# Optimization experiments

Hardware: AMD Instinct MI355X
Metric: run time of the kernel (lower is better)

## Reference

```python
import jax, jax.numpy as jnp
import numpy as np

N_ROLES = 6
EPS = 1e-5

def _ln(x, scale, bias):
    m = jnp.mean(x, axis=-1, keepdims=True)
    v = jnp.var(x, axis=-1, keepdims=True)
    return (x - m) * jax.lax.rsqrt(v + EPS) * scale + bias

def setup_inputs() -> dict:
    key = jax.random.key(0)
    ks = jax.random.split(key, 20)
    T, B, D_OBS, H, A = 32, 1024, 256, 512, 32
    inp = {
        'rnn_states': jax.random.normal(ks[0], (B, H), jnp.float32),
        'obs': jax.random.normal(ks[1], (T, B, D_OBS), jnp.float32),
        'resets': jnp.zeros((T, B), jnp.float32),
        'available_actions': jnp.ones((T, B, A), jnp.float32),
        'role_ids': jax.random.randint(ks[2], (T, B), 0, N_ROLES, jnp.int32),
        # feature norm over obs_dim
        'fn_scale': jnp.ones((D_OBS,), jnp.float32),
        'fn_bias': jnp.zeros((D_OBS,), jnp.float32),
        # base MLP: obs_dim->512->512, each followed by LayerNorm
        'W0': jax.random.normal(ks[3], (D_OBS, H), jnp.float32) * 0.02,
        'b0': jnp.zeros((H,), jnp.float32),
        'ln0_scale': jnp.ones((H,), jnp.float32),
        'ln0_bias': jnp.zeros((H,), jnp.float32),
        'W1': jax.random.normal(ks[4], (H, H), jnp.float32) * 0.02,
        'b1': jnp.zeros((H,), jnp.float32),
        'ln1_scale': jnp.ones((H,), jnp.float32),
        'ln1_bias': jnp.zeros((H,), jnp.float32),
        # per-role routes: obs_dim->128->H (stacked over roles)
        'Wr0': jax.random.normal(ks[5], (N_ROLES, D_OBS, 128), jnp.float32) * 0.02,
        'br0': jnp.zeros((N_ROLES, 128), jnp.float32),
        'Wr1': jax.random.normal(ks[6], (N_ROLES, 128, H), jnp.float32) * 0.02,
        'br1': jnp.zeros((N_ROLES, H), jnp.float32),
        # per-role heads: H->64->32->action_dim (stacked over roles)
        'Wh0': jax.random.normal(ks[7], (N_ROLES, H, 64), jnp.float32) * 0.02,
        'bh0': jnp.zeros((N_ROLES, 64), jnp.float32),
        'Wh1': jax.random.normal(ks[8], (N_ROLES, 64, 32), jnp.float32) * 0.02,
        'bh1': jnp.zeros((N_ROLES, 32), jnp.float32),
        'Wh2': jax.random.normal(ks[9], (N_ROLES, 32, A), jnp.float32) * 0.02,
        'bh2': jnp.zeros((N_ROLES, A), jnp.float32),
    }
    return inp

def _gather_by_role(all_values, role_ids):
    # all_values: (K, T, B, F); role_ids: (T, B) -> (T, B, F)
    idx = role_ids[None, :, :, None].astype(jnp.int32)
    return jnp.take_along_axis(all_values, idx, axis=0)[0]

def reference(rnn_states, obs, resets, available_actions, role_ids,
              fn_scale, fn_bias, W0, b0, ln0_scale, ln0_bias,
              W1, b1, ln1_scale, ln1_bias,
              Wr0, br0, Wr1, br1,
              Wh0, bh0, Wh1, bh1, Wh2, bh2):
    # feature normalization on raw obs
    obs_n = _ln(obs, fn_scale, fn_bias)
    # shared base MLP (relu + LayerNorm after each Dense)
    e = _ln(jax.nn.relu(obs_n @ W0 + b0), ln0_scale, ln0_bias)
    e = _ln(jax.nn.relu(e @ W1 + b1), ln1_scale, ln1_bias)
    # per-role pre-GRU residual routes on (normalized) obs
    r = jax.nn.relu(jnp.einsum('tbi,kih->ktbh', obs_n, Wr0) + br0[:, None, None, :])
    r = jax.nn.relu(jnp.einsum('ktbh,kho->ktbo', r, Wr1) + br1[:, None, None, :])
    e = e + _gather_by_role(r, role_ids)
    # no recurrent policy configured: rnn_states pass through
    # per-role heads -> all logits (K, T, B, A)
    h = jax.nn.relu(jnp.einsum('tbh,khf->ktbf', e, Wh0) + bh0[:, None, None, :])
    h = jax.nn.relu(jnp.einsum('ktbf,kfg->ktbg', h, Wh1) + bh1[:, None, None, :])
    all_logits = jnp.einsum('ktbg,kga->ktba', h, Wh2) + bh2[:, None, None, :]
    logits = _gather_by_role(all_logits, role_ids)
    logits = jnp.where(available_actions > 0.5, logits, jnp.full_like(logits, -1e10))
    return rnn_states, logits
```

## Files before the change

kernel.cpp:

```cpp
#include <hip/hip_runtime.h>
#include <stdint.h>

typedef unsigned short u16;
typedef unsigned int u32;

using bf16x8 = __attribute__((ext_vector_type(8))) short;
using f32x4  = __attribute__((ext_vector_type(4))) float;

#define DEVINL __device__ __forceinline__

DEVINL float b2f(u16 u) { return __builtin_bit_cast(float, (u32)u << 16); }
DEVINL u16 f2b(float f) {
  u32 u = __builtin_bit_cast(u32, f);
  u += 0x7FFFu + ((u >> 16) & 1u);
  return (u16)(u >> 16);
}

DEVINL void gll16(const u16* src, u16* dst) {
  __builtin_amdgcn_global_load_lds(
      (const __attribute__((address_space(1))) void*)(uintptr_t)src,
      (__attribute__((address_space(3))) void*)(uintptr_t)dst, 16, 0, 0);
}

#define MFMA __builtin_amdgcn_mfma_f32_16x16x32_bf16

DEVINL void tp_tile(const float* __restrict__ s, u16* __restrict__ d,
                    int R, int C, int bx, int by, int z)
{
  __shared__ u16 tile[32][33];
  const size_t mstride = (size_t)R * C;
  s += (size_t)z * mstride;
  d += (size_t)z * mstride;
  int r0 = bx * 32, c0 = by * 32;
  int tx = threadIdx.x & 31, ty = threadIdx.x >> 5;
#pragma unroll
  for (int i = 0; i < 32; i += 8)
    tile[ty + i][tx] = f2b(s[(size_t)(r0 + ty + i) * C + (c0 + tx)]);
  __syncthreads();
#pragma unroll
  for (int i = 0; i < 32; i += 8)
    d[(size_t)(c0 + ty + i) * R + (r0 + tx)] = tile[tx][ty + i];
}

__global__ __launch_bounds__(256) void transpose_all(
    const float* W0, const float* W1, const float* Wr0, const float* Wr1, const float* Wh0,
    u16* W0t, u16* W1t, u16* Wr0t, u16* Wr1t, u16* Wh0t)
{
  int b = blockIdx.x;
  if (b < 128)      {            tp_tile(W0, W0t, 256, 512, b % 8,  b / 8, 0); }
  else if (b < 384) { b -= 128;  tp_tile(W1, W1t, 512, 512, b % 16, b / 16, 0); }
  else if (b < 576) { b -= 384;  int t = b / 8;  tp_tile(Wr0, Wr0t, 256, 128, b % 8,  t % 4,  t / 4); }
  else if (b < 960) { b -= 576;  int t = b / 4;  tp_tile(Wr1, Wr1t, 128, 512, b % 4,  t % 16, t / 16); }
  else              { b -= 960;  int t = b / 16; tp_tile(Wh0, Wh0t, 512, 64,  b % 16, t % 2,  t / 2); }
}

__global__ __launch_bounds__(256) void ln_f32_256(
    const float* __restrict__ X, const float* __restrict__ sc,
    const float* __restrict__ bi, u16* __restrict__ Y, int nrows)
{
  constexpr int D = 256, PER = 4;
  int lane = threadIdx.x & 63;
  int row = blockIdx.x * 4 + (threadIdx.x >> 6);
  if (row >= nrows) return;
  const float* xr = X + (size_t)row * D + lane * PER;
  float x[PER] __attribute__((aligned(16)));
  *(float4*)x = *(const float4*)xr;
  float s = 0.f, s2 = 0.f;
#pragma unroll
  for (int p = 0; p < PER; ++p) { s += x[p]; s2 += x[p] * x[p]; }
#pragma unroll
  for (int o = 32; o > 0; o >>= 1) { s += __shfl_xor(s, o, 64); s2 += __shfl_xor(s2, o, 64); }
  float m = s * (1.f / D);
  float v = s2 * (1.f / D) - m * m;
  float inv = rsqrtf(v + 1e-5f);
  u16 yu[PER] __attribute__((aligned(8)));
#pragma unroll
  for (int p = 0; p < PER; ++p)
    yu[p] = f2b((x[p] - m) * inv * sc[lane * PER + p] + bi[lane * PER + p]);
  *(uint2*)(Y + (size_t)row * D + lane * PER) = *(uint2*)yu;
}

#define NROLE 6
__global__ __launch_bounds__(256) void role_count(
    const int* __restrict__ rid, int* __restrict__ blkCnt)
{
  __shared__ int h[NROLE];
  if (threadIdx.x < NROLE) h[threadIdx.x] = 0;
  __syncthreads();
  int i = blockIdx.x * 256 + threadIdx.x;
  atomicAdd(&h[rid[i]], 1);
  __syncthreads();
  if (threadIdx.x < NROLE) blkCnt[blockIdx.x * NROLE + threadIdx.x] = h[threadIdx.x];
}

__global__ __launch_bounds__(256) void role_scan(
    const int* __restrict__ blkCnt, int* __restrict__ blkBase,
    int* __restrict__ baseArr, int* __restrict__ cntArr)
{
  __shared__ int c[128 * NROLE];
  __shared__ int bb[128 * NROLE];
  __shared__ int sbase[NROLE], scnt[NROLE];
  for (int i = threadIdx.x; i < 128 * NROLE; i += 256) c[i] = blkCnt[i];
  __syncthreads();
  if (threadIdx.x < NROLE) {
    int k = threadIdx.x, run = 0;
    for (int b = 0; b < 128; ++b) { bb[b * NROLE + k] = run; run += c[b * NROLE + k]; }
    scnt[k] = run;
  }
  __syncthreads();
  if (threadIdx.x == 0) {
    int r = 0;
    for (int k = 0; k < NROLE; ++k) { sbase[k] = r; r += scnt[k]; }
  }
  __syncthreads();
  if (threadIdx.x < NROLE) { baseArr[threadIdx.x] = sbase[threadIdx.x]; cntArr[threadIdx.x] = scnt[threadIdx.x]; }
  for (int i = threadIdx.x; i < 128 * NROLE; i += 256)
    blkBase[i] = bb[i] + sbase[i % NROLE];
}

__global__ __launch_bounds__(256) void role_fill(
    const int* __restrict__ rid, const int* __restrict__ blkBase, int* __restrict__ bucket)
{
  __shared__ int h[NROLE];
  if (threadIdx.x < NROLE) h[threadIdx.x] = 0;
  __syncthreads();
  int i = blockIdx.x * 256 + threadIdx.x;
  int k = rid[i];
  int pos = atomicAdd(&h[k], 1);
  bucket[blkBase[blockIdx.x * NROLE + k] + pos] = i;
}

template <int K>
__global__ __launch_bounds__(256, 2) void gemm_ln(
    const u16* __restrict__ A, const u16* __restrict__ Bt,
    const float* __restrict__ bias, const float* __restrict__ lnsc,
    const float* __restrict__ lnbi, u16* __restrict__ C)
{
  constexpr int BK = 64, NI = K / BK;
  __shared__ __align__(16) u16 As[2][64 * BK];
  __shared__ float redS[64][4];
  __shared__ float redSS[64][4];
  __shared__ float prm[1536];
  const int tid = threadIdx.x;
  const int rowBase = blockIdx.x * 64;
  const int lane = tid & 63, wave = tid >> 6;
#pragma unroll
  for (int i = tid; i < 512; i += 256) {
    prm[i] = bias[i]; prm[512 + i] = lnsc[i]; prm[1024 + i] = lnbi[i];
  }
  u32 aOff[2];
#pragma unroll
  for (int r = 0; r < 2; ++r) {
    int row = r * 32 + (tid >> 3);
    aOff[r] = (u32)(rowBase + row) * (u32)K + (u32)(((tid & 7) ^ (row & 7)) * 8);
  }
  const int quad = lane >> 4, lm = lane & 15, l7 = lm & 7;
  const int wn = wave * 128;
  u32 bOff[8];
#pragma unroll
  for (int j = 0; j < 8; ++j)
    bOff[j] = (u32)(wn + j * 16 + lm) * (u32)K + (u32)(quad * 8);

  f32x4 acc[4][8] = {};

#pragma unroll
  for (int r = 0; r < 2; ++r)
    gll16(A + aOff[r], &As[0][r * 2048 + wave * 512]);
  bf16x8 bP[8];
#pragma unroll
  for (int j = 0; j < 8; ++j)
    bP[j] = *(const bf16x8*)(Bt + bOff[j]);
  __syncthreads();

  for (int i = 0; i < NI; ++i) {
    const u16* Ab = As[i & 1];
    if (i + 1 < NI) {
#pragma unroll
      for (int r = 0; r < 2; ++r)
        gll16(A + aOff[r] + (i + 1) * BK, &As[(i + 1) & 1][r * 2048 + wave * 512]);
    }
    bf16x8 bN[8];
#pragma unroll
    for (int j = 0; j < 8; ++j)
      bN[j] = *(const bf16x8*)(Bt + bOff[j] + i * BK + 32);
    bf16x8 af[4];
#pragma unroll
    for (int i2 = 0; i2 < 4; ++i2)
      af[i2] = *(const bf16x8*)&Ab[(i2 * 16 + lm) * 64 + ((quad ^ l7) * 8)];
#pragma unroll
    for (int i2 = 0; i2 < 4; ++i2)
#pragma unroll
      for (int j = 0; j < 8; ++j)
        acc[i2][j] = MFMA(af[i2], bP[j], acc[i2][j], 0, 0, 0);
    if (i + 1 < NI) {
#pragma unroll
      for (int j = 0; j < 8; ++j)
        bP[j] = *(const bf16x8*)(Bt + bOff[j] + (i + 1) * BK);
    }
#pragma unroll
    for (int i2 = 0; i2 < 4; ++i2)
      af[i2] = *(const bf16x8*)&Ab[(i2 * 16 + lm) * 64 + (((quad + 4) ^ l7) * 8)];
#pragma unroll
    for (int i2 = 0; i2 < 4; ++i2)
#pragma unroll
      for (int j = 0; j < 8; ++j)
        acc[i2][j] = MFMA(af[i2], bN[j], acc[i2][j], 0, 0, 0);
    __syncthreads();
  }

#pragma unroll
  for (int i2 = 0; i2 < 4; ++i2) {
#pragma unroll
    for (int r2 = 0; r2 < 4; ++r2) {
      float s = 0.f, ss = 0.f;
#pragma unroll
      for (int j = 0; j < 8; ++j) {
        float v = fmaxf(acc[i2][j][r2] + prm[wn + j * 16 + lm], 0.f);
        acc[i2][j][r2] = v;
        s += v; ss += v * v;
      }
#pragma unroll
      for (int o = 1; o < 16; o <<= 1) { s += __shfl_xor(s, o, 64); ss += __shfl_xor(ss, o, 64); }
      if (lm == 0) {
        int rowL = i2 * 16 + quad * 4 + r2;
        redS[rowL][wave] = s;
        redSS[rowL][wave] = ss;
      }
    }
  }
  __syncthreads();
#pragma unroll
  for (int i2 = 0; i2 < 4; ++i2) {
#pragma unroll
    for (int r2 = 0; r2 < 4; ++r2) {
      int rowL = i2 * 16 + quad * 4 + r2;
      float ts  = redS[rowL][0] + redS[rowL][1] + redS[rowL][2] + redS[rowL][3];
      float tss = redSS[rowL][0] + redSS[rowL][1] + redSS[rowL][2] + redSS[rowL][3];
      float m = ts * (1.f / 512.f);
      float var = tss * (1.f / 512.f) - m * m;
      float inv = rsqrtf(var + 1e-5f);
      size_t base = (size_t)(rowBase + rowL) * 512;
#pragma unroll
      for (int j = 0; j < 8; ++j) {
        int col = wn + j * 16 + lm;
        float y = (acc[i2][j][r2] - m) * inv * prm[512 + col] + prm[1024 + col];
        C[base + col] = f2b(y);
      }
    }
  }
}

__global__ __launch_bounds__(256, 2) void route_head(
    const u16* __restrict__ obs_n, const u16* __restrict__ e,
    const u16* __restrict__ Wr0t, const float* __restrict__ br0,
    const u16* __restrict__ Wr1t, const float* __restrict__ br1,
    const u16* __restrict__ Wh0t, const float* __restrict__ bh0,
    const float* __restrict__ Wh1, const float* __restrict__ bh1,
    const float* __restrict__ Wh2, const float* __restrict__ bh2,
    const float* __restrict__ avail,
    const int* __restrict__ bucket, const int* __restrict__ baseArr,
    const int* __restrict__ cntArr, float* __restrict__ outLogits)
{
  __shared__ __align__(16) u16 sm[28672];
  __shared__ float prm[704];
  __shared__ float h1s[32 * 36];
  const int tid = threadIdx.x;

  int role = 0, rem = blockIdx.x, cnt;
  for (;;) {
    cnt = cntArr[role];
    int tiles = (cnt + 31) >> 5;
    if (rem < tiles) break;
    rem -= tiles;
    if (++role >= NROLE) return;
  }
  const int limit = cnt;
  const int rowBase = rem * 32;
  const int roleBase = baseArr[role];

  const int lane = tid & 63, wave = tid >> 6;
  const int quad = lane >> 4, lm = lane & 15, l7 = lm & 7;

#pragma unroll
  for (int r = 0; r < 4; ++r) {
    int lrow = r * 8 + (tid >> 5);
    int i = rowBase + lrow;
    if (i >= limit) i = rowBase;
    int grow = bucket[roleBase + i];
    gll16(obs_n + (u32)grow * 256u + (u32)(((tid & 31) ^ (lrow & 7)) * 8),
          &sm[16384 + r * 2048 + wave * 512]);
  }
#pragma unroll
  for (int r = 0; r < 8; ++r) {
    int lrow = r * 4 + wave;
    int i = rowBase + lrow;
    if (i >= limit) i = rowBase;
    int grow = bucket[roleBase + i];
    int chunk = tid & 63;
    int sw = (chunk & 56) | ((chunk ^ lrow) & 7);
    gll16(e + (u32)grow * 512u + (u32)(sw * 8),
          &sm[r * 2048 + wave * 512]);
  }
  {
    if (tid < 128) prm[tid] = br0[role * 128 + tid];
    for (int i = tid; i < 512; i += 256) prm[128 + i] = br1[role * 512 + i];
    if (tid < 64) prm[640 + tid] = bh0[role * 64 + tid];
  }
  __syncthreads();

  const int wn0 = wave * 32;
  const u16* B0 = Wr0t + (size_t)role * 128 * 256;
  f32x4 acc0[2][2] = {};
  bf16x8 b0P[2];
#pragma unroll
  for (int j = 0; j < 2; ++j)
    b0P[j] = *(const bf16x8*)(B0 + (u32)(wn0 + j * 16 + lm) * 256u + (u32)(quad * 8));
#pragma unroll
  for (int kk = 0; kk < 256; kk += 32) {
    bf16x8 b0N[2];
    if (kk + 32 < 256) {
#pragma unroll
      for (int j = 0; j < 2; ++j)
        b0N[j] = *(const bf16x8*)(B0 + (u32)(wn0 + j * 16 + lm) * 256u + (u32)(quad * 8 + kk + 32));
    }
    const int kc = kk >> 3;
    bf16x8 af[2];
#pragma unroll
    for (int i2 = 0; i2 < 2; ++i2)
      af[i2] = *(const bf16x8*)&sm[16384 + (i2 * 16 + lm) * 256 + (((quad + kc) ^ l7) * 8)];
#pragma unroll
    for (int i2 = 0; i2 < 2; ++i2)
#pragma unroll
      for (int j = 0; j < 2; ++j)
        acc0[i2][j] = MFMA(af[i2], b0P[j], acc0[i2][j], 0, 0, 0);
    if (kk + 32 < 256) { b0P[0] = b0N[0]; b0P[1] = b0N[1]; }
  }
  u16* r1 = sm + 24576;
#pragma unroll
  for (int i2 = 0; i2 < 2; ++i2) {
#pragma unroll
    for (int r2 = 0; r2 < 4; ++r2) {
      int row = i2 * 16 + quad * 4 + r2;
#pragma unroll
      for (int j = 0; j < 2; ++j) {
        int col = wn0 + j * 16 + lm;
        float v = fmaxf(acc0[i2][j][r2] + prm[col], 0.f);
        r1[row * 128 + (((col >> 3) ^ (row & 7)) * 8) + (col & 7)] = f2b(v);
      }
    }
  }
  __syncthreads();

  const int wn1 = wave * 128;
  const u16* B1 = Wr1t + (size_t)role * 512 * 128;
  f32x4 acc1[2][8] = {};
  bf16x8 b1P[8];
#pragma unroll
  for (int j = 0; j < 8; ++j)
    b1P[j] = *(const bf16x8*)(B1 + (u32)(wn1 + j * 16 + lm) * 128u + (u32)(quad * 8));
#pragma unroll
  for (int kk = 0; kk < 128; kk += 32) {
    bf16x8 b1N[8];
    if (kk + 32 < 128) {
#pragma unroll
      for (int j = 0; j < 8; ++j)
        b1N[j] = *(const bf16x8*)(B1 + (u32)(wn1 + j * 16 + lm) * 128u + (u32)(quad * 8 + kk + 32));
    }
    const int kc = kk >> 3;
    bf16x8 af[2];
#pragma unroll
    for (int i2 = 0; i2 < 2; ++i2)
      af[i2] = *(const bf16x8*)&r1[(i2 * 16 + lm) * 128 + (((quad + kc) ^ l7) * 8)];
#pragma unroll
    for (int i2 = 0; i2 < 2; ++i2)
#pragma unroll
      for (int j = 0; j < 8; ++j)
        acc1[i2][j] = MFMA(af[i2], b1P[j], acc1[i2][j], 0, 0, 0);
    if (kk + 32 < 128) {
#pragma unroll
      for (int j = 0; j < 8; ++j) b1P[j] = b1N[j];
    }
  }
#pragma unroll
  for (int i2 = 0; i2 < 2; ++i2) {
#pragma unroll
    for (int r2 = 0; r2 < 4; ++r2) {
      int row = i2 * 16 + quad * 4 + r2;
#pragma unroll
      for (int j = 0; j < 8; ++j) {
        int col = wn1 + j * 16 + lm;
        int addr = row * 512 + (((col >> 3) ^ (row & 7)) * 8) + (col & 7);
        float v = fmaxf(acc1[i2][j][r2] + prm[128 + col], 0.f) + b2f(sm[addr]);
        sm[addr] = f2b(v);
      }
    }
  }
  __syncthreads();

  const int wn2 = wave * 16;
  const u16* B2 = Wh0t + (size_t)role * 64 * 512;
  f32x4 acc2[2] = {};
  bf16x8 b2P = *(const bf16x8*)(B2 + (u32)(wn2 + lm) * 512u + (u32)(quad * 8));
#pragma unroll
  for (int kk = 0; kk < 512; kk += 32) {
    bf16x8 b2N;
    if (kk + 32 < 512)
      b2N = *(const bf16x8*)(B2 + (u32)(wn2 + lm) * 512u + (u32)(quad * 8 + kk + 32));
    const int kc = kk >> 3;
    bf16x8 af[2];
#pragma unroll
    for (int i2 = 0; i2 < 2; ++i2)
      af[i2] = *(const bf16x8*)&sm[(i2 * 16 + lm) * 512 + (((quad + kc) ^ l7) * 8)];
#pragma unroll
    for (int i2 = 0; i2 < 2; ++i2)
      acc2[i2] = MFMA(af[i2], b2P, acc2[i2], 0, 0, 0);
    if (kk + 32 < 512) b2P = b2N;
  }
  u16* h0s = sm + 16384;
#pragma unroll
  for (int i2 = 0; i2 < 2; ++i2) {
#pragma unroll
    for (int r2 = 0; r2 < 4; ++r2) {
      int row = i2 * 16 + quad * 4 + r2;
      int col = wn2 + lm;
      h0s[row * 68 + col] = f2b(fmaxf(acc2[i2][r2] + prm[640 + col], 0.f));
    }
  }
  __syncthreads();

  {
    const int r = tid >> 3;
    const int n0 = (tid & 7) * 4;
    const bool valid = (rowBase + r) < limit;
    const float* W1k = Wh1 + (size_t)role * 64 * 32;
    const float* W2k = Wh2 + (size_t)role * 32 * 32;
    float4 a1 = *(const float4*)(bh1 + role * 32 + n0);
#pragma unroll 8
    for (int j = 0; j < 64; ++j) {
      float hj = b2f(h0s[r * 68 + j]);
      float4 wv = *(const float4*)(W1k + j * 32 + n0);
      a1.x += hj * wv.x; a1.y += hj * wv.y; a1.z += hj * wv.z; a1.w += hj * wv.w;
    }
    h1s[r * 36 + n0 + 0] = fmaxf(a1.x, 0.f);
    h1s[r * 36 + n0 + 1] = fmaxf(a1.y, 0.f);
    h1s[r * 36 + n0 + 2] = fmaxf(a1.z, 0.f);
    h1s[r * 36 + n0 + 3] = fmaxf(a1.w, 0.f);
    __syncthreads();
    float4 a2 = *(const float4*)(bh2 + role * 32 + n0);
#pragma unroll 8
    for (int n = 0; n < 32; ++n) {
      float hn = h1s[r * 36 + n];
      float4 wv = *(const float4*)(W2k + n * 32 + n0);
      a2.x += hn * wv.x; a2.y += hn * wv.y; a2.z += hn * wv.z; a2.w += hn * wv.w;
    }
    if (valid) {
      int g = bucket[roleBase + rowBase + r];
      float4 av = *(const float4*)(avail + (size_t)g * 32 + n0);
      float4 o;
      o.x = (av.x > 0.5f) ? a2.x : -1e10f;
      o.y = (av.y > 0.5f) ? a2.y : -1e10f;
      o.z = (av.z > 0.5f) ? a2.z : -1e10f;
      o.w = (av.w > 0.5f) ? a2.w : -1e10f;
      *(float4*)(outLogits + (size_t)g * 32 + n0) = o;
    }
  }
}

extern "C" void kernel_launch(void* const* d_in, const int* in_sizes, int n_in,
                              void* d_out, int out_size, void* d_ws, size_t ws_size,
                              hipStream_t stream)
{
  const float* rnn  = (const float*)d_in[0];
  const float* obs  = (const float*)d_in[1];
  const float* avail= (const float*)d_in[3];
  const int*   rid  = (const int*)d_in[4];
  const float* fn_s = (const float*)d_in[5];
  const float* fn_b = (const float*)d_in[6];
  const float* W0   = (const float*)d_in[7];
  const float* b0   = (const float*)d_in[8];
  const float* ln0s = (const float*)d_in[9];
  const float* ln0b = (const float*)d_in[10];
  const float* W1   = (const float*)d_in[11];
  const float* b1   = (const float*)d_in[12];
  const float* ln1s = (const float*)d_in[13];
  const float* ln1b = (const float*)d_in[14];
  const float* Wr0  = (const float*)d_in[15];
  const float* br0  = (const float*)d_in[16];
  const float* Wr1  = (const float*)d_in[17];
  const float* br1  = (const float*)d_in[18];
  const float* Wh0  = (const float*)d_in[19];
  const float* bh0  = (const float*)d_in[20];
  const float* Wh1  = (const float*)d_in[21];
  const float* bh1  = (const float*)d_in[22];
  const float* Wh2  = (const float*)d_in[23];
  const float* bh2  = (const float*)d_in[24];

  const int ROWS = 32768;

  char* w = (char*)d_ws;
  auto carve = [&](size_t bytes) { char* p = w; w += (bytes + 255) & ~(size_t)255; return p; };
  u16* obs_n  = (u16*)carve((size_t)ROWS * 256 * 2);
  u16* bufA   = (u16*)carve((size_t)ROWS * 512 * 2);
  u16* bufB   = (u16*)carve((size_t)ROWS * 512 * 2);
  u16* W0t    = (u16*)carve((size_t)512 * 256 * 2);
  u16* W1t    = (u16*)carve((size_t)512 * 512 * 2);
  u16* Wr0t   = (u16*)carve((size_t)6 * 128 * 256 * 2);
  u16* Wr1t   = (u16*)carve((size_t)6 * 512 * 128 * 2);
  u16* Wh0t   = (u16*)carve((size_t)6 * 64 * 512 * 2);
  int* bucket = (int*)carve((size_t)ROWS * 4);
  int* blkCnt = (int*)carve((size_t)128 * NROLE * 4);
  int* blkBase= (int*)carve((size_t)128 * NROLE * 4);
  int* baseArr= (int*)carve(256);
  int* cntArr = (int*)carve(256);

  float* outLogits = (float*)d_out + (size_t)1024 * 512;

  hipMemcpyAsync(d_out, rnn, (size_t)1024 * 512 * 4, hipMemcpyDeviceToDevice, stream);

  transpose_all<<<1152, 256, 0, stream>>>(W0, W1, Wr0, Wr1, Wh0, W0t, W1t, Wr0t, Wr1t, Wh0t);

  ln_f32_256<<<8192, 256, 0, stream>>>(obs, fn_s, fn_b, obs_n, ROWS);

  role_count<<<128, 256, 0, stream>>>(rid, blkCnt);
  role_scan<<<1, 256, 0, stream>>>(blkCnt, blkBase, baseArr, cntArr);
  role_fill<<<128, 256, 0, stream>>>(rid, blkBase, bucket);

  gemm_ln<256><<<512, 256, 0, stream>>>(obs_n, W0t, b0, ln0s, ln0b, bufA);
  gemm_ln<512><<<512, 256, 0, stream>>>(bufA, W1t, b1, ln1s, ln1b, bufB);

  route_head<<<1029, 256, 0, stream>>>(obs_n, bufB, Wr0t, br0, Wr1t, br1, Wh0t, bh0,
                                       Wh1, bh1, Wh2, bh2, avail,
                                       bucket, baseArr, cntArr, outLogits);
}
```

Measured before the change: 280.6 us.

## Fuse preprocessing kernels into one launch and raise route_head occupancy

Result: faster. 267.5 us (-4.7%).

```diff
diff --git a/kernel.cpp b/kernel.cpp
--- a/kernel.cpp
+++ b/kernel.cpp
@@ -23,6 +23,7 @@
 }
 
 #define MFMA __builtin_amdgcn_mfma_f32_16x16x32_bf16
+#define NROLE 6
 
 DEVINL void tp_tile(const float* __restrict__ s, u16* __restrict__ d,
                     int R, int C, int bx, int by, int z)
@@ -42,92 +43,90 @@
     d[(size_t)(c0 + ty + i) * R + (r0 + tx)] = tile[tx][ty + i];
 }
 
-__global__ __launch_bounds__(256) void transpose_all(
+__global__ __launch_bounds__(256) void mega0(
     const float* W0, const float* W1, const float* Wr0, const float* Wr1, const float* Wh0,
-    u16* W0t, u16* W1t, u16* Wr0t, u16* Wr1t, u16* Wh0t)
+    u16* W0t, u16* W1t, u16* Wr0t, u16* Wr1t, u16* Wh0t,
+    const float* __restrict__ obs, const float* __restrict__ fn_s,
+    const float* __restrict__ fn_b, u16* __restrict__ obs_n,
+    const int* __restrict__ rid, int* __restrict__ blkCnt,
+    const float* __restrict__ rnn, float* __restrict__ outRnn)
 {
   int b = blockIdx.x;
-  if (b < 128)      {            tp_tile(W0, W0t, 256, 512, b % 8,  b / 8, 0); }
-  else if (b < 384) { b -= 128;  tp_tile(W1, W1t, 512, 512, b % 16, b / 16, 0); }
-  else if (b < 576) { b -= 384;  int t = b / 8;  tp_tile(Wr0, Wr0t, 256, 128, b % 8,  t % 4,  t / 4); }
-  else if (b < 960) { b -= 576;  int t = b / 4;  tp_tile(Wr1, Wr1t, 128, 512, b % 4,  t % 16, t / 16); }
-  else              { b -= 960;  int t = b / 16; tp_tile(Wh0, Wh0t, 512, 64,  b % 16, t % 2,  t / 2); }
-}
-
-__global__ __launch_bounds__(256) void ln_f32_256(
-    const float* __restrict__ X, const float* __restrict__ sc,
-    const float* __restrict__ bi, u16* __restrict__ Y, int nrows)
-{
-  constexpr int D = 256, PER = 4;
-  int lane = threadIdx.x & 63;
-  int row = blockIdx.x * 4 + (threadIdx.x >> 6);
-  if (row >= nrows) return;
-  const float* xr = X + (size_t)row * D + lane * PER;
-  float x[PER] __attribute__((aligned(16)));
-  *(float4*)x = *(const float4*)xr;
-  float s = 0.f, s2 = 0.f;
-#pragma unroll
-  for (int p = 0; p < PER; ++p) { s += x[p]; s2 += x[p] * x[p]; }
-#pragma unroll
-  for (int o = 32; o > 0; o >>= 1) { s += __shfl_xor(s, o, 64); s2 += __shfl_xor(s2, o, 64); }
-  float m = s * (1.f / D);
-  float v = s2 * (1.f / D) - m * m;
-  float inv = rsqrtf(v + 1e-5f);
-  u16 yu[PER] __attribute__((aligned(8)));
-#pragma unroll
-  for (int p = 0; p < PER; ++p)
-    yu[p] = f2b((x[p] - m) * inv * sc[lane * PER + p] + bi[lane * PER + p]);
-  *(uint2*)(Y + (size_t)row * D + lane * PER) = *(uint2*)yu;
-}
-
-#define NROLE 6
-__global__ __launch_bounds__(256) void role_count(
-    const int* __restrict__ rid, int* __restrict__ blkCnt)
-{
-  __shared__ int h[NROLE];
-  if (threadIdx.x < NROLE) h[threadIdx.x] = 0;
-  __syncthreads();
-  int i = blockIdx.x * 256 + threadIdx.x;
-  atomicAdd(&h[rid[i]], 1);
-  __syncthreads();
-  if (threadIdx.x < NROLE) blkCnt[blockIdx.x * NROLE + threadIdx.x] = h[threadIdx.x];
-}
-
-__global__ __launch_bounds__(256) void role_scan(
-    const int* __restrict__ blkCnt, int* __restrict__ blkBase,
-    int* __restrict__ baseArr, int* __restrict__ cntArr)
+  const int tid = threadIdx.x;
+  if (b < 1152) {
+    if (b < 128)      {            tp_tile(W0, W0t, 256, 512, b % 8,  b / 8, 0); }
+    else if (b < 384) { b -= 128;  tp_tile(W1, W1t, 512, 512, b % 16, b / 16, 0); }
+    else if (b < 576) { b -= 384;  int t = b / 8;  tp_tile(Wr0, Wr0t, 256, 128, b % 8,  t % 4,  t / 4); }
+    else if (b < 960) { b -= 576;  int t = b / 4;  tp_tile(Wr1, Wr1t, 128, 512, b % 4,  t % 16, t / 16); }
+    else              { b -= 960;  int t = b / 16; tp_tile(Wh0, Wh0t, 512, 64,  b % 16, t % 2,  t / 2); }
+  } else if (b < 3200) {
+    b -= 1152;
+    const int lane = tid & 63, wave = tid >> 6;
+#pragma unroll
+    for (int it = 0; it < 4; ++it) {
+      int row = b * 16 + wave * 4 + it;
+      const float* xr = obs + (size_t)row * 256 + lane * 4;
+      float x[4] __attribute__((aligned(16)));
+      *(float4*)x = *(const float4*)xr;
+      float s = 0.f, s2 = 0.f;
+#pragma unroll
+      for (int p = 0; p < 4; ++p) { s += x[p]; s2 += x[p] * x[p]; }
+#pragma unroll
+      for (int o = 32; o > 0; o >>= 1) { s += __shfl_xor(s, o, 64); s2 += __shfl_xor(s2, o, 64); }
+      float m = s * (1.f / 256.f);
+      float v = s2 * (1.f / 256.f) - m * m;
+      float inv = rsqrtf(v + 1e-5f);
+      u16 yu[4] __attribute__((aligned(8)));
+#pragma unroll
+      for (int p = 0; p < 4; ++p)
+        yu[p] = f2b((x[p] - m) * inv * fn_s[lane * 4 + p] + fn_b[lane * 4 + p]);
+      *(uint2*)(obs_n + (size_t)row * 256 + lane * 4) = *(uint2*)yu;
+    }
+  } else if (b < 3328) {
+    b -= 3200;
+    __shared__ int h[NROLE];
+    if (tid < NROLE) h[tid] = 0;
+    __syncthreads();
+    atomicAdd(&h[rid[b * 256 + tid]], 1);
+    __syncthreads();
+    if (tid < NROLE) blkCnt[b * NROLE + tid] = h[tid];
+  } else {
+    b -= 3328;
+    const float4* src = (const float4*)rnn;
+    float4* dst = (float4*)outRnn;
+    int base = (b * 256 + tid) * 4;
+#pragma unroll
+    for (int i = 0; i < 4; ++i) dst[base + i] = src[base + i];
+  }
+}
+
+__global__ __launch_bounds__(256) void fill2(
+    const int* __restrict__ rid, const int* __restrict__ blkCnt,
+    int* __restrict__ bucket, int* __restrict__ baseArr, int* __restrict__ cntArr)
 {
   __shared__ int c[128 * NROLE];
-  __shared__ int bb[128 * NROLE];
-  __shared__ int sbase[NROLE], scnt[NROLE];
-  for (int i = threadIdx.x; i < 128 * NROLE; i += 256) c[i] = blkCnt[i];
-  __syncthreads();
-  if (threadIdx.x < NROLE) {
-    int k = threadIdx.x, run = 0;
-    for (int b = 0; b < 128; ++b) { bb[b * NROLE + k] = run; run += c[b * NROLE + k]; }
-    scnt[k] = run;
-  }
-  __syncthreads();
-  if (threadIdx.x == 0) {
+  __shared__ int preArr[NROLE], scnt[NROLE], sbase[NROLE], h[NROLE];
+  const int tid = threadIdx.x;
+  const int bx = blockIdx.x;
+  for (int i = tid; i < 128 * NROLE; i += 256) c[i] = blkCnt[i];
+  if (tid < NROLE) h[tid] = 0;
+  __syncthreads();
+  if (tid < NROLE) {
+    int k = tid, run = 0, pre = 0;
+    for (int b = 0; b < 128; ++b) { if (b == bx) pre = run; run += c[b * NROLE + k]; }
+    scnt[k] = run; preArr[k] = pre;
+  }
+  __syncthreads();
+  if (tid == 0) {
     int r = 0;
     for (int k = 0; k < NROLE; ++k) { sbase[k] = r; r += scnt[k]; }
   }
   __syncthreads();
-  if (threadIdx.x < NROLE) { baseArr[threadIdx.x] = sbase[threadIdx.x]; cntArr[threadIdx.x] = scnt[threadIdx.x]; }
-  for (int i = threadIdx.x; i < 128 * NROLE; i += 256)
-    blkBase[i] = bb[i] + sbase[i % NROLE];
-}
-
-__global__ __launch_bounds__(256) void role_fill(
-    const int* __restrict__ rid, const int* __restrict__ blkBase, int* __restrict__ bucket)
-{
-  __shared__ int h[NROLE];
-  if (threadIdx.x < NROLE) h[threadIdx.x] = 0;
-  __syncthreads();
-  int i = blockIdx.x * 256 + threadIdx.x;
+  if (bx == 0 && tid < NROLE) { baseArr[tid] = sbase[tid]; cntArr[tid] = scnt[tid]; }
+  int i = bx * 256 + tid;
   int k = rid[i];
   int pos = atomicAdd(&h[k], 1);
-  bucket[blkBase[blockIdx.x * NROLE + k] + pos] = i;
+  bucket[sbase[k] + preArr[k] + pos] = i;
 }
 
 template <int K>
@@ -250,7 +249,7 @@
   }
 }
 
-__global__ __launch_bounds__(256, 2) void route_head(
+__global__ __launch_bounds__(256, 3) void route_head(
     const u16* __restrict__ obs_n, const u16* __restrict__ e,
     const u16* __restrict__ Wr0t, const float* __restrict__ br0,
     const u16* __restrict__ Wr1t, const float* __restrict__ br1,
@@ -261,9 +260,8 @@
     const int* __restrict__ bucket, const int* __restrict__ baseArr,
     const int* __restrict__ cntArr, float* __restrict__ outLogits)
 {
-  __shared__ __align__(16) u16 sm[28672];
+  __shared__ __align__(16) u16 sm[24960];
   __shared__ float prm[704];
-  __shared__ float h1s[32 * 36];
   const int tid = threadIdx.x;
 
   int role = 0, rem = blockIdx.x, cnt;
@@ -298,8 +296,7 @@
     int grow = bucket[roleBase + i];
     int chunk = tid & 63;
     int sw = (chunk & 56) | ((chunk ^ lrow) & 7);
-    gll16(e + (u32)grow * 512u + (u32)(sw * 8),
-          &sm[r * 2048 + wave * 512]);
+    gll16(e + (u32)grow * 512u + (u32)(sw * 8), &sm[r * 2048 + wave * 512]);
   }
   {
     if (tid < 128) prm[tid] = br0[role * 128 + tid];
@@ -311,31 +308,33 @@
   const int wn0 = wave * 32;
   const u16* B0 = Wr0t + (size_t)role * 128 * 256;
   f32x4 acc0[2][2] = {};
-  bf16x8 b0P[2];
-#pragma unroll
-  for (int j = 0; j < 2; ++j)
-    b0P[j] = *(const bf16x8*)(B0 + (u32)(wn0 + j * 16 + lm) * 256u + (u32)(quad * 8));
-#pragma unroll
-  for (int kk = 0; kk < 256; kk += 32) {
-    bf16x8 b0N[2];
-    if (kk + 32 < 256) {
+  bf16x8 b0R[2][2];
+#pragma unroll
+  for (int p = 0; p < 2; ++p)
+#pragma unroll
+    for (int j = 0; j < 2; ++j)
+      b0R[p][j] = *(const bf16x8*)(B0 + (u32)(wn0 + j * 16 + lm) * 256u + (u32)(quad * 8 + p * 32));
+#pragma unroll
+  for (int it = 0; it < 8; ++it) {
+    bf16x8 cur0 = b0R[it & 1][0], cur1 = b0R[it & 1][1];
+    if (it + 2 < 8) {
 #pragma unroll
       for (int j = 0; j < 2; ++j)
-        b0N[j] = *(const bf16x8*)(B0 + (u32)(wn0 + j * 16 + lm) * 256u + (u32)(quad * 8 + kk + 32));
-    }
-    const int kc = kk >> 3;
+        b0R[it & 1][j] = *(const bf16x8*)(B0 + (u32)(wn0 + j * 16 + lm) * 256u + (u32)(quad * 8 + (it + 2) * 32));
+    }
+    const int kc = it * 4;
     bf16x8 af[2];
 #pragma unroll
     for (int i2 = 0; i2 < 2; ++i2)
       af[i2] = *(const bf16x8*)&sm[16384 + (i2 * 16 + lm) * 256 + (((quad + kc) ^ l7) * 8)];
 #pragma unroll
-    for (int i2 = 0; i2 < 2; ++i2)
-#pragma unroll
-      for (int j = 0; j < 2; ++j)
-        acc0[i2][j] = MFMA(af[i2], b0P[j], acc0[i2][j], 0, 0, 0);
-    if (kk + 32 < 256) { b0P[0] = b0N[0]; b0P[1] = b0N[1]; }
-  }
-  u16* r1 = sm + 24576;
+    for (int i2 = 0; i2 < 2; ++i2) {
+      acc0[i2][0] = MFMA(af[i2], cur0, acc0[i2][0], 0, 0, 0);
+      acc0[i2][1] = MFMA(af[i2], cur1, acc0[i2][1], 0, 0, 0);
+    }
+  }
+  __syncthreads();
+  u16* r1 = sm + 16384;
 #pragma unroll
   for (int i2 = 0; i2 < 2; ++i2) {
 #pragma unroll
@@ -400,23 +399,25 @@
   const int wn2 = wave * 16;
   const u16* B2 = Wh0t + (size_t)role * 64 * 512;
   f32x4 acc2[2] = {};
-  bf16x8 b2P = *(const bf16x8*)(B2 + (u32)(wn2 + lm) * 512u + (u32)(quad * 8));
-#pragma unroll
-  for (int kk = 0; kk < 512; kk += 32) {
-    bf16x8 b2N;
-    if (kk + 32 < 512)
-      b2N = *(const bf16x8*)(B2 + (u32)(wn2 + lm) * 512u + (u32)(quad * 8 + kk + 32));
-    const int kc = kk >> 3;
+  bf16x8 b2R[4];
+#pragma unroll
+  for (int p = 0; p < 4; ++p)
+    b2R[p] = *(const bf16x8*)(B2 + (u32)(wn2 + lm) * 512u + (u32)(quad * 8 + p * 32));
+#pragma unroll
+  for (int it = 0; it < 16; ++it) {
+    bf16x8 cur = b2R[it & 3];
+    if (it + 4 < 16)
+      b2R[it & 3] = *(const bf16x8*)(B2 + (u32)(wn2 + lm) * 512u + (u32)(quad * 8 + (it + 4) * 32));
+    const int kc = it * 4;
     bf16x8 af[2];
 #pragma unroll
     for (int i2 = 0; i2 < 2; ++i2)
       af[i2] = *(const bf16x8*)&sm[(i2 * 16 + lm) * 512 + (((quad + kc) ^ l7) * 8)];
 #pragma unroll
     for (int i2 = 0; i2 < 2; ++i2)
-      acc2[i2] = MFMA(af[i2], b2P, acc2[i2], 0, 0, 0);
-    if (kk + 32 < 512) b2P = b2N;
-  }
-  u16* h0s = sm + 16384;
+      acc2[i2] = MFMA(af[i2], cur, acc2[i2], 0, 0, 0);
+  }
+  u16* h0s = sm + 20480;
 #pragma unroll
   for (int i2 = 0; i2 < 2; ++i2) {
 #pragma unroll
@@ -429,6 +430,7 @@
   __syncthreads();
 
   {
+    float* h1s = (float*)&sm[22656];
     const int r = tid >> 3;
     const int n0 = (tid & 7) * 4;
     const bool valid = (rowBase + r) < limit;
@@ -509,21 +511,15 @@
   u16* Wh0t   = (u16*)carve((size_t)6 * 64 * 512 * 2);
   int* bucket = (int*)carve((size_t)ROWS * 4);
   int* blkCnt = (int*)carve((size_t)128 * NROLE * 4);
-  int* blkBase= (int*)carve((size_t)128 * NROLE * 4);
   int* baseArr= (int*)carve(256);
   int* cntArr = (int*)carve(256);
 
   float* outLogits = (float*)d_out + (size_t)1024 * 512;
 
-  hipMemcpyAsync(d_out, rnn, (size_t)1024 * 512 * 4, hipMemcpyDeviceToDevice, stream);
-
-  transpose_all<<<1152, 256, 0, stream>>>(W0, W1, Wr0, Wr1, Wh0, W0t, W1t, Wr0t, Wr1t, Wh0t);
-
-  ln_f32_256<<<8192, 256, 0, stream>>>(obs, fn_s, fn_b, obs_n, ROWS);
-
-  role_count<<<128, 256, 0, stream>>>(rid, blkCnt);
-  role_scan<<<1, 256, 0, stream>>>(blkCnt, blkBase, baseArr, cntArr);
-  role_fill<<<128, 256, 0, stream>>>(rid, blkBase, bucket);
+  mega0<<<3456, 256, 0, stream>>>(W0, W1, Wr0, Wr1, Wh0, W0t, W1t, Wr0t, Wr1t, Wh0t,
+                                  obs, fn_s, fn_b, obs_n, rid, blkCnt, rnn, (float*)d_out);
+
+  fill2<<<128, 256, 0, stream>>>(rid, blkCnt, bucket, baseArr, cntArr);
 
   gemm_ln<256><<<512, 256, 0, stream>>>(obs_n, W0t, b0, ln0s, ln0b, bufA);
   gemm_ln<512><<<512, 256, 0, stream>>>(bufA, W1t, b1, ln1s, ln1b, bufB);
```
